# Kernel optimization log

Measured on AMD Instinct MI355X. Metric: run time of the kernel, lower is better.

The kernel has to match this reference:

```python
import jax, jax.numpy as jnp
import numpy as np


def setup_inputs() -> dict:
    key = jax.random.key(0)
    k0, k1, k2, k3 = jax.random.split(key, 4)
    B, C_IN, H, W = 8, 256, 64, 64
    O, NUM = 256, 8  # output channels, number of regions
    mat0 = jax.random.normal(k0, (B, C_IN, H, W), dtype=jnp.float32)
    mat1 = jax.random.normal(k1, (O, C_IN, NUM), dtype=jnp.float32)  # per-region 1x1 filters (shared across batch, batch_W=1)
    mask = jax.random.uniform(k2, (NUM, H, W), dtype=jnp.float32)    # soft region weights per pixel
    Alpha = jax.random.uniform(k3, (NUM,), dtype=jnp.float32)        # per-region modulation scale
    return {"mat0": mat0, "mat1": mat1, "mask": mask, "Alpha": Alpha, "use_alpha": 1, "beta": 1}


def reference(mat0, mat1, mask, Alpha, use_alpha, beta):
    # Deformable (region-aware) matmul: for each pixel (h,w), apply the
    # region-r filter mat1[:, :, r] to mat0[:, :, h, w], weighted by the
    # per-pixel soft region mask (optionally alpha-modulated per region).
    # out[b,o,h,w] = sum_r sum_c mat0[b,c,h,w] * mat1[o,c,r] * Alpha[r] * mask[r,h,w]
    m1 = mat1 * Alpha if use_alpha else mat1  # [O, C, R] scaled per region
    return jnp.einsum('bchw,ocr,rhw->bohw', mat0, m1, mask)
```

## Files before the change

kernel.cpp:

```cpp
#include <hip/hip_runtime.h>
#include <hip/hip_bf16.h>
#include <stdint.h>


typedef __attribute__((ext_vector_type(8)))  _Float16 half8;
typedef __attribute__((ext_vector_type(16))) float    f32x16;

#define C_IN  256
#define HW_   4096
#define NRND  32

__global__ __launch_bounds__(256) void prep_w_kernel(
    const float* __restrict__ mat1, const float* __restrict__ Alpha,
    const int* __restrict__ use_alpha, _Float16* __restrict__ Aprep) {
  int t = blockIdx.x * 256 + threadIdx.x;
  int o = t & 255;
  int c = t >> 8;
  int ua = use_alpha[0];
  const float* src = mat1 + ((size_t)o * C_IN + c) * 8;
  half8 v;
#pragma unroll
  for (int r = 0; r < 8; ++r) {
    float s = ua ? Alpha[r] : 1.0f;
    v[r] = (_Float16)(src[r] * s);
  }
  *(half8*)(Aprep + ((size_t)c * 256 + o) * 8) = v;
}

__global__ __launch_bounds__(256, 2) void gemm_deform_kernel(
    const float* __restrict__ mat0, const _Float16* __restrict__ Aprep,
    const float* __restrict__ mask, float* __restrict__ out) {
  __shared__ half8 A_lds[2][1024];

  int bid = blockIdx.x;
  int wg = (bid & 7) * 64 + (bid >> 3);
  int tile_m = wg & 1;
  int tile_n = wg >> 1;
  int o0 = tile_m * 128;
  int n0 = tile_n * 128;
  int b  = n0 >> 12;
  int p0 = n0 & 4095;

  int t    = threadIdx.x;
  int lane = t & 63;
  int w    = t >> 6;
  int wc   = w & 1;
  int wr   = w >> 1;
  int l31  = lane & 31;
  int cr   = lane >> 5;

  int colb = p0 + wc * 64 + l31;
  half8 mkh[2];
#pragma unroll
  for (int ni = 0; ni < 2; ++ni)
#pragma unroll
    for (int r = 0; r < 8; ++r)
      mkh[ni][r] = (_Float16)mask[r * HW_ + colb + ni * 32];

  const float* __restrict__ m0b =
      mat0 + ((size_t)b * C_IN + cr) * HW_ + colb;

  const __attribute__((address_space(1))) uint32_t* gA =
      (const __attribute__((address_space(1))) uint32_t*)Aprep;
  __attribute__((address_space(3))) uint32_t* lA =
      (__attribute__((address_space(3))) uint32_t*)&A_lds[0][0];
  int soo  = (w & 1) * 64 + lane;
  int scqb = w >> 1;

  f32x16 acc[2][2];
#pragma unroll
  for (int mi = 0; mi < 2; ++mi)
#pragma unroll
    for (int ni = 0; ni < 2; ++ni)
#pragma unroll
      for (int j = 0; j < 16; ++j) acc[mi][ni][j] = 0.f;

  float P[4][2];

#pragma unroll
  for (int i = 0; i < 4; ++i) {
    int gslot = (0 * 8 + i * 2 + scqb) * 256 + o0 + soo;
    __builtin_amdgcn_global_load_lds(gA + (size_t)gslot * 4,
                                     lA + (size_t)(i * 256 + w * 64) * 4,
                                     16, 0, 0);
  }
#pragma unroll
  for (int kq = 0; kq < 4; ++kq) {
    P[kq][0] = m0b[(size_t)(kq * 2) * HW_];
    P[kq][1] = m0b[(size_t)(kq * 2) * HW_ + 32];
  }
  asm volatile("s_waitcnt vmcnt(8)" ::: "memory");
  __builtin_amdgcn_s_barrier();

#pragma unroll 1
  for (int rd = 0; rd < NRND; ++rd) {
    const half8* __restrict__ Abuf = &A_lds[rd & 1][0];
    int bufn = (rd & 1) ^ 1;
    int rs = rd + 1 > 31 ? 31 : rd + 1;
    int gbase = rs * 8;
#pragma unroll
    for (int p = 0; p < 4; ++p) {
      int gslot = (gbase + p * 2 + scqb) * 256 + o0 + soo;
      __builtin_amdgcn_global_load_lds(gA + (size_t)gslot * 4,
                                       lA + (size_t)(bufn * 1024 + p * 256 + w * 64) * 4,
                                       16, 0, 0);
      half8 a0 = Abuf[(p * 2 + cr) * 128 + wr * 64 + l31];
      half8 a1 = Abuf[(p * 2 + cr) * 128 + wr * 64 + 32 + l31];
      __builtin_amdgcn_s_barrier();
      _Float16 h0 = (_Float16)P[p][0];
      _Float16 h1 = (_Float16)P[p][1];
      half8 pb0 = {h0, h0, h0, h0, h0, h0, h0, h0};
      half8 pb1 = {h1, h1, h1, h1, h1, h1, h1, h1};
      half8 bv0 = pb0 * mkh[0];
      half8 bv1 = pb1 * mkh[1];
      __builtin_amdgcn_s_setprio(1);
      acc[0][0] = __builtin_amdgcn_mfma_f32_32x32x16_f16(a0, bv0, acc[0][0], 0, 0, 0);
      acc[0][1] = __builtin_amdgcn_mfma_f32_32x32x16_f16(a0, bv1, acc[0][1], 0, 0, 0);
      acc[1][0] = __builtin_amdgcn_mfma_f32_32x32x16_f16(a1, bv0, acc[1][0], 0, 0, 0);
      acc[1][1] = __builtin_amdgcn_mfma_f32_32x32x16_f16(a1, bv1, acc[1][1], 0, 0, 0);
      __builtin_amdgcn_s_setprio(0);
      const float* mnext = m0b + (size_t)(gbase + p * 2) * HW_;
      P[p][0] = mnext[0];
      P[p][1] = mnext[32];
    }
    asm volatile("s_waitcnt vmcnt(2)" ::: "memory");
    __builtin_amdgcn_s_barrier();
  }

  size_t obase = (size_t)b * 256 * HW_ + colb;
#pragma unroll
  for (int mi = 0; mi < 2; ++mi) {
#pragma unroll
    for (int ni = 0; ni < 2; ++ni) {
#pragma unroll
      for (int reg = 0; reg < 16; ++reg) {
        int row = o0 + wr * 64 + mi * 32 + (reg & 3) + 8 * (reg >> 2) + 4 * cr;
        out[obase + (size_t)row * HW_ + ni * 32] = acc[mi][ni][reg];
      }
    }
  }
}

extern "C" void kernel_launch(void* const* d_in, const int* in_sizes, int n_in,
                              void* d_out, int out_size, void* d_ws, size_t ws_size,
                              hipStream_t stream) {
  const float* mat0      = (const float*)d_in[0];
  const float* mat1      = (const float*)d_in[1];
  const float* mask      = (const float*)d_in[2];
  const float* Alpha     = (const float*)d_in[3];
  const int*   use_alpha = (const int*)d_in[4];
  (void)in_sizes; (void)n_in; (void)out_size; (void)ws_size;

  _Float16* Aprep = (_Float16*)d_ws;
  float* outp  = (float*)d_out;

  prep_w_kernel<<<256, 256, 0, stream>>>(mat1, Alpha, use_alpha, Aprep);
  gemm_deform_kernel<<<512, 256, 0, stream>>>(mat0, Aprep, mask, outp);
}
```

Baseline: 50.68 us.

## Quad-buffer weight LDS staging and cut per-step barriers in deform GEMM

The LDS buffer for the prepared weights grows from two to four slabs, and the main loop is restructured to process two rounds per barrier phase instead of one. This removes the barrier that previously sat inside each inner k-step. Staging pointers are hoisted and incremented instead of being recomputed each time. The mat0 scalar prefetches are split into even and odd register sets so loads run further ahead. The cost is double the LDS footprint (64KB per block), which could limit occupancy to two blocks per CU. A full vmcnt(0) wait now precedes each barrier.

After: 47.98 us. 1.06x faster.

```diff
diff --git a/kernel.cpp b/kernel.cpp
--- a/kernel.cpp
+++ b/kernel.cpp
@@ -30,7 +30,7 @@
 __global__ __launch_bounds__(256, 2) void gemm_deform_kernel(
     const float* __restrict__ mat0, const _Float16* __restrict__ Aprep,
     const float* __restrict__ mask, float* __restrict__ out) {
-  __shared__ half8 A_lds[2][1024];
+  __shared__ half8 A_lds[4][1024];
 
   int bid = blockIdx.x;
   int wg = (bid & 7) * 64 + (bid >> 3);
@@ -50,12 +50,12 @@
   int cr   = lane >> 5;
 
   int colb = p0 + wc * 64 + l31;
-  half8 mkh[2];
+  half8 mkh0, mkh1;
 #pragma unroll
-  for (int ni = 0; ni < 2; ++ni)
-#pragma unroll
-    for (int r = 0; r < 8; ++r)
-      mkh[ni][r] = (_Float16)mask[r * HW_ + colb + ni * 32];
+  for (int r = 0; r < 8; ++r) {
+    mkh0[r] = (_Float16)mask[r * HW_ + colb];
+    mkh1[r] = (_Float16)mask[r * HW_ + colb + 32];
+  }
 
   const float* __restrict__ m0b =
       mat0 + ((size_t)b * C_IN + cr) * HW_ + colb;
@@ -66,78 +66,114 @@
       (__attribute__((address_space(3))) uint32_t*)&A_lds[0][0];
   int soo  = (w & 1) * 64 + lane;
   int scqb = w >> 1;
+  const __attribute__((address_space(1))) uint32_t* gS0 =
+      gA + (size_t)((0 * 2 + scqb) * 256 + o0 + soo) * 4;
+  const __attribute__((address_space(1))) uint32_t* gS1 =
+      gA + (size_t)((1 * 2 + scqb) * 256 + o0 + soo) * 4;
+  const __attribute__((address_space(1))) uint32_t* gS2 =
+      gA + (size_t)((2 * 2 + scqb) * 256 + o0 + soo) * 4;
+  const __attribute__((address_space(1))) uint32_t* gS3 =
+      gA + (size_t)((3 * 2 + scqb) * 256 + o0 + soo) * 4;
+  const float* pP0 = m0b + (size_t)0 * HW_;
+  const float* pP1 = m0b + (size_t)2 * HW_;
+  const float* pP2 = m0b + (size_t)4 * HW_;
+  const float* pP3 = m0b + (size_t)6 * HW_;
 
-  f32x16 acc[2][2];
+#define STAGE(SLAB, SB) do {                                                  \
+    __builtin_amdgcn_global_load_lds(gS0, lA + ((SLAB)*1024 + 0*256 + w*64)*4, 16, 0, 0); \
+    __builtin_amdgcn_global_load_lds(gS1, lA + ((SLAB)*1024 + 1*256 + w*64)*4, 16, 0, 0); \
+    __builtin_amdgcn_global_load_lds(gS2, lA + ((SLAB)*1024 + 2*256 + w*64)*4, 16, 0, 0); \
+    __builtin_amdgcn_global_load_lds(gS3, lA + ((SLAB)*1024 + 3*256 + w*64)*4, 16, 0, 0); \
+    gS0 += (SB); gS1 += (SB); gS2 += (SB); gS3 += (SB);                       \
+  } while (0)
+
+  f32x16 acc00, acc01, acc10, acc11;
 #pragma unroll
-  for (int mi = 0; mi < 2; ++mi)
-#pragma unroll
-    for (int ni = 0; ni < 2; ++ni)
-#pragma unroll
-      for (int j = 0; j < 16; ++j) acc[mi][ni][j] = 0.f;
+  for (int j = 0; j < 16; ++j) { acc00[j] = 0.f; acc01[j] = 0.f; acc10[j] = 0.f; acc11[j] = 0.f; }
 
-  float P[4][2];
+  float Pev[4][2], Pod[4][2];
 
-#pragma unroll
-  for (int i = 0; i < 4; ++i) {
-    int gslot = (0 * 8 + i * 2 + scqb) * 256 + o0 + soo;
-    __builtin_amdgcn_global_load_lds(gA + (size_t)gslot * 4,
-                                     lA + (size_t)(i * 256 + w * 64) * 4,
-                                     16, 0, 0);
-  }
-#pragma unroll
-  for (int kq = 0; kq < 4; ++kq) {
-    P[kq][0] = m0b[(size_t)(kq * 2) * HW_];
-    P[kq][1] = m0b[(size_t)(kq * 2) * HW_ + 32];
-  }
-  asm volatile("s_waitcnt vmcnt(8)" ::: "memory");
-  __builtin_amdgcn_s_barrier();
+  auto SM = [&](float s0, float s1, half8 A0, half8 A1) {
+    _Float16 h0 = (_Float16)s0, h1 = (_Float16)s1;
+    half8 pb0 = {h0, h0, h0, h0, h0, h0, h0, h0};
+    half8 pb1 = {h1, h1, h1, h1, h1, h1, h1, h1};
+    half8 bv0 = pb0 * mkh0;
+    half8 bv1 = pb1 * mkh1;
+    acc00 = __builtin_amdgcn_mfma_f32_32x32x16_f16(A0, bv0, acc00, 0, 0, 0);
+    acc01 = __builtin_amdgcn_mfma_f32_32x32x16_f16(A0, bv1, acc01, 0, 0, 0);
+    acc10 = __builtin_amdgcn_mfma_f32_32x32x16_f16(A1, bv0, acc10, 0, 0, 0);
+    acc11 = __builtin_amdgcn_mfma_f32_32x32x16_f16(A1, bv1, acc11, 0, 0, 0);
+  };
+
+  int abase = wr * 64 + l31;
+
+  auto COMP = [&](const half8* __restrict__ Ab, float (&P)[4][2], int PB) {
+    half8 a0 = Ab[(0 + cr) * 128 + abase];
+    half8 a1 = Ab[(0 + cr) * 128 + abase + 32];
+    half8 b0 = Ab[(2 + cr) * 128 + abase];
+    half8 b1 = Ab[(2 + cr) * 128 + abase + 32];
+    SM(P[0][0], P[0][1], a0, a1);
+    P[0][0] = pP0[0]; P[0][1] = pP0[32]; pP0 += PB;
+    a0 = Ab[(4 + cr) * 128 + abase];
+    a1 = Ab[(4 + cr) * 128 + abase + 32];
+    SM(P[1][0], P[1][1], b0, b1);
+    P[1][0] = pP1[0]; P[1][1] = pP1[32]; pP1 += PB;
+    b0 = Ab[(6 + cr) * 128 + abase];
+    b1 = Ab[(6 + cr) * 128 + abase + 32];
+    SM(P[2][0], P[2][1], a0, a1);
+    P[2][0] = pP2[0]; P[2][1] = pP2[32]; pP2 += PB;
+    SM(P[3][0], P[3][1], b0, b1);
+    P[3][0] = pP3[0]; P[3][1] = pP3[32]; pP3 += PB;
+  };
+
+  STAGE(0, 8192);
+  STAGE(1, 8192);
+  Pev[0][0] = pP0[0]; Pev[0][1] = pP0[32]; pP0 += 8 * HW_;
+  Pev[1][0] = pP1[0]; Pev[1][1] = pP1[32]; pP1 += 8 * HW_;
+  Pev[2][0] = pP2[0]; Pev[2][1] = pP2[32]; pP2 += 8 * HW_;
+  Pev[3][0] = pP3[0]; Pev[3][1] = pP3[32]; pP3 += 8 * HW_;
+  Pod[0][0] = pP0[0]; Pod[0][1] = pP0[32]; pP0 += 8 * HW_;
+  Pod[1][0] = pP1[0]; Pod[1][1] = pP1[32]; pP1 += 8 * HW_;
+  Pod[2][0] = pP2[0]; Pod[2][1] = pP2[32]; pP2 += 8 * HW_;
+  Pod[3][0] = pP3[0]; Pod[3][1] = pP3[32]; pP3 += 8 * HW_;
 
 #pragma unroll 1
-  for (int rd = 0; rd < NRND; ++rd) {
-    const half8* __restrict__ Abuf = &A_lds[rd & 1][0];
-    int bufn = (rd & 1) ^ 1;
-    int rs = rd + 1 > 31 ? 31 : rd + 1;
-    int gbase = rs * 8;
-#pragma unroll
-    for (int p = 0; p < 4; ++p) {
-      int gslot = (gbase + p * 2 + scqb) * 256 + o0 + soo;
-      __builtin_amdgcn_global_load_lds(gA + (size_t)gslot * 4,
-                                       lA + (size_t)(bufn * 1024 + p * 256 + w * 64) * 4,
-                                       16, 0, 0);
-      half8 a0 = Abuf[(p * 2 + cr) * 128 + wr * 64 + l31];
-      half8 a1 = Abuf[(p * 2 + cr) * 128 + wr * 64 + 32 + l31];
-      __builtin_amdgcn_s_barrier();
-      _Float16 h0 = (_Float16)P[p][0];
-      _Float16 h1 = (_Float16)P[p][1];
-      half8 pb0 = {h0, h0, h0, h0, h0, h0, h0, h0};
-      half8 pb1 = {h1, h1, h1, h1, h1, h1, h1, h1};
-      half8 bv0 = pb0 * mkh[0];
-      half8 bv1 = pb1 * mkh[1];
-      __builtin_amdgcn_s_setprio(1);
-      acc[0][0] = __builtin_amdgcn_mfma_f32_32x32x16_f16(a0, bv0, acc[0][0], 0, 0, 0);
-      acc[0][1] = __builtin_amdgcn_mfma_f32_32x32x16_f16(a0, bv1, acc[0][1], 0, 0, 0);
-      acc[1][0] = __builtin_amdgcn_mfma_f32_32x32x16_f16(a1, bv0, acc[1][0], 0, 0, 0);
-      acc[1][1] = __builtin_amdgcn_mfma_f32_32x32x16_f16(a1, bv1, acc[1][1], 0, 0, 0);
-      __builtin_amdgcn_s_setprio(0);
-      const float* mnext = m0b + (size_t)(gbase + p * 2) * HW_;
-      P[p][0] = mnext[0];
-      P[p][1] = mnext[32];
+  for (int g = 0; g < 8; ++g) {
+    int rd = g * 4;
+    asm volatile("s_waitcnt vmcnt(0)" ::: "memory");
+    __builtin_amdgcn_s_barrier();
+    {
+      int sb2 = (rd + 2 < 31) ? 8192 : 0;
+      int sb3 = (rd + 3 < 31) ? 8192 : 0;
+      int pb2 = (rd + 2 < 31) ? 8 * HW_ : 0;
+      int pb3 = (rd + 3 < 31) ? 8 * HW_ : 0;
+      STAGE(2, sb2);
+      STAGE(3, sb3);
+      COMP(&A_lds[0][0], Pev, pb2);
+      COMP(&A_lds[1][0], Pod, pb3);
     }
-    asm volatile("s_waitcnt vmcnt(2)" ::: "memory");
+    asm volatile("s_waitcnt vmcnt(0)" ::: "memory");
     __builtin_amdgcn_s_barrier();
+    {
+      int sb4 = (rd + 4 < 31) ? 8192 : 0;
+      int sb5 = (rd + 5 < 31) ? 8192 : 0;
+      int pb4 = (rd + 4 < 31) ? 8 * HW_ : 0;
+      int pb5 = (rd + 5 < 31) ? 8 * HW_ : 0;
+      STAGE(0, sb4);
+      STAGE(1, sb5);
+      COMP(&A_lds[2][0], Pev, pb4);
+      COMP(&A_lds[3][0], Pod, pb5);
+    }
   }
 
   size_t obase = (size_t)b * 256 * HW_ + colb;
 #pragma unroll
-  for (int mi = 0; mi < 2; ++mi) {
-#pragma unroll
-    for (int ni = 0; ni < 2; ++ni) {
-#pragma unroll
-      for (int reg = 0; reg < 16; ++reg) {
-        int row = o0 + wr * 64 + mi * 32 + (reg & 3) + 8 * (reg >> 2) + 4 * cr;
-        out[obase + (size_t)row * HW_ + ni * 32] = acc[mi][ni][reg];
-      }
-    }
+  for (int reg = 0; reg < 16; ++reg) {
+    int row = o0 + wr * 64 + (reg & 3) + 8 * (reg >> 2) + 4 * cr;
+    out[obase + (size_t)row * HW_]                    = acc00[reg];
+    out[obase + (size_t)row * HW_ + 32]               = acc01[reg];
+    out[obase + (size_t)(row + 32) * HW_]             = acc10[reg];
+    out[obase + (size_t)(row + 32) * HW_ + 32]        = acc11[reg];
   }
 }
 
```
